# Optimization experiments

Measured on AMD Instinct MI355X. Metric: run time of the kernel, lower is better.

## Reference

```python
import jax, jax.numpy as jnp
import numpy as np

NUM_HEADS = 4
NUM_GROUPS = 8
EPS = 1e-5


def setup_inputs() -> dict:
    key = jax.random.key(0)
    ks = jax.random.split(key, 4)
    b, c, h, w = 16, 512, 32, 32
    x = jax.random.normal(ks[0], (b, c, h, w), dtype=jnp.float32)
    norm_gamma = jnp.ones((c,), dtype=jnp.float32)
    norm_beta = jnp.zeros((c,), dtype=jnp.float32)
    qkv_w = jax.random.normal(ks[1], (3 * c, c), dtype=jnp.float32) * (c ** -0.5)
    qkv_b = jnp.zeros((3 * c,), dtype=jnp.float32)
    proj_w = jax.random.normal(ks[2], (c, c), dtype=jnp.float32) * (c ** -0.5)
    proj_b = jnp.zeros((c,), dtype=jnp.float32)
    return {"x": x, "norm_gamma": norm_gamma, "norm_beta": norm_beta,
            "qkv_w": qkv_w, "qkv_b": qkv_b, "proj_w": proj_w, "proj_b": proj_b}


def reference(x, norm_gamma, norm_beta, qkv_w, qkv_b, proj_w, proj_b):
    b, c, h, w = x.shape
    nh = NUM_HEADS
    dh = c // nh
    n = h * w
    # GroupNorm(8, c): normalize over (c/G, h, w) within each group, biased var
    xg = x.reshape(b, NUM_GROUPS, -1)
    mu = jnp.mean(xg, axis=-1, keepdims=True)
    var = jnp.var(xg, axis=-1, keepdims=True)
    xn = ((xg - mu) * jax.lax.rsqrt(var + EPS)).reshape(b, c, h, w)
    xn = xn * norm_gamma[:, None, None] + norm_beta[:, None, None]
    # QKV 1x1 conv == channel matmul
    qkv = jnp.einsum('oc,bchw->bohw', qkv_w, xn) + qkv_b[:, None, None]
    q, k, v = jnp.split(qkv, 3, axis=1)  # each [b, c, h, w]

    def to_heads(t):  # [b, c, h, w] -> [b, nh, n, dh]
        return t.reshape(b, nh, dh, n).transpose(0, 1, 3, 2)

    q, k, v = to_heads(q), to_heads(k), to_heads(v)
    scale = dh ** -0.5
    attn = jax.nn.softmax(jnp.einsum('bhnd,bhmd->bhnm', q, k) * scale, axis=-1)
    out = jnp.einsum('bhnm,bhmd->bhnd', attn, v)  # [b, nh, n, dh]
    out = out.transpose(0, 1, 3, 2).reshape(b, c, h, w)
    out = jnp.einsum('oc,bchw->bohw', proj_w, out) + proj_b[:, None, None]
    return x + out
```

## Files before the change

kernel.cpp:

```cpp
#include <hip/hip_runtime.h>

typedef unsigned short u16;
typedef unsigned int   u32;

typedef __attribute__((ext_vector_type(8)))  short bf16x8;
typedef __attribute__((ext_vector_type(16))) float f32x16;
typedef __attribute__((ext_vector_type(2)))  unsigned int u32x2;
#define MFMA32(a, b, c) __builtin_amdgcn_mfma_f32_32x32x16_bf16(a, b, c, 0, 0, 0)

__device__ __forceinline__ float bf2f(u16 h) { return __uint_as_float(((u32)h) << 16); }
__device__ __forceinline__ u16 f2bf(float f) {
  u32 u = __float_as_uint(f);
  u += 0x7fffu + ((u >> 16) & 1u);
  return (u16)(u >> 16);
}
__device__ __forceinline__ void unpack8(uint4 u, float* f) {
  f[0] = __uint_as_float(u.x << 16); f[1] = __uint_as_float(u.x & 0xffff0000u);
  f[2] = __uint_as_float(u.y << 16); f[3] = __uint_as_float(u.y & 0xffff0000u);
  f[4] = __uint_as_float(u.z << 16); f[5] = __uint_as_float(u.z & 0xffff0000u);
  f[6] = __uint_as_float(u.w << 16); f[7] = __uint_as_float(u.w & 0xffff0000u);
}
__device__ __forceinline__ void unpack4(uint2 u, float* f) {
  f[0] = __uint_as_float(u.x << 16); f[1] = __uint_as_float(u.x & 0xffff0000u);
  f[2] = __uint_as_float(u.y << 16); f[3] = __uint_as_float(u.y & 0xffff0000u);
}

template <bool F>
__device__ __forceinline__ void load8(const void* p, size_t idx, float* f) {
  if constexpr (F) {
    const float4* q = (const float4*)((const float*)p + idx);
    float4 a = q[0], b = q[1];
    f[0] = a.x; f[1] = a.y; f[2] = a.z; f[3] = a.w;
    f[4] = b.x; f[5] = b.y; f[6] = b.z; f[7] = b.w;
  } else {
    unpack8(*(const uint4*)((const u16*)p + idx), f);
  }
}
template <bool F>
__device__ __forceinline__ void load4(const void* p, size_t idx, float* f) {
  if constexpr (F) {
    float4 a = *(const float4*)((const float*)p + idx);
    f[0] = a.x; f[1] = a.y; f[2] = a.z; f[3] = a.w;
  } else {
    unpack4(*(const uint2*)((const u16*)p + idx), f);
  }
}
template <bool F>
__device__ __forceinline__ float load1(const void* p, size_t idx) {
  if constexpr (F) return ((const float*)p)[idx];
  else return bf2f(((const u16*)p)[idx]);
}

__device__ __forceinline__ void gl2lds16(const void* g, void* l) {
  __builtin_amdgcn_global_load_lds(
      (const __attribute__((address_space(1))) void*)g,
      (__attribute__((address_space(3))) void*)l, 16, 0, 0);
}

__global__ void detect_dtype(const void* __restrict__ x, int* __restrict__ flag) {
  if (threadIdx.x == 0 && blockIdx.x == 0) {
    const u32* p = (const u32*)x;
    int sane = 0;
    for (int i = 0; i < 256; ++i) {
      u32 e = (p[i] >> 7) & 0xFFu;
      sane += (e >= 100u && e <= 150u) ? 1 : 0;
    }
    *flag = (sane < 192) ? 1 : 0;
  }
}

__global__ void signal_ws(u16* __restrict__ out, int n) {
  int i = blockIdx.x * 256 + threadIdx.x;
  if (i < n) out[i] = 0x42C8;
}

#define SM_SCALE 0.08838834764831843f
#define QSC 0.12751743f


template <bool F>
__global__ void __launch_bounds__(256) wconv(const void* __restrict__ qkvw,
                                             const void* __restrict__ qkvb,
                                             u16* __restrict__ dst,
                                             const int* __restrict__ flag) {
  if ((flag[0] != 0) != F) return;
  int i = blockIdx.x * 256 + threadIdx.x;
  if (i < 786432) {
    dst[i] = F ? f2bf(((const float*)qkvw)[i]) : ((const u16*)qkvw)[i];
  } else if (i < 787968) {
    int j = i - 786432;
    dst[i] = F ? f2bf(((const float*)qkvb)[j]) : ((const u16*)qkvb)[j];
  }
}

template <bool F>
__global__ void __launch_bounds__(256) gn_norm(const void* __restrict__ x,
                                               const void* __restrict__ gamma,
                                               const void* __restrict__ beta,
                                               u16* __restrict__ xT,
                                               const int* __restrict__ flag) {
  if ((flag[0] != 0) != F) return;
  const int g = blockIdx.x, b = blockIdx.y;
  const int tid = threadIdx.x;
  const size_t base = (size_t)(b * 512 + g * 64) * 1024;
  float sum = 0.f, sq = 0.f;
  for (int i = tid; i < 8192; i += 256) {
    float f[8]; load8<F>(x, base + (size_t)i * 8, f);
#pragma unroll
    for (int m = 0; m < 8; ++m) { sum += f[m]; sq += f[m] * f[m]; }
  }
  __shared__ float ssum[256], ssq[256];
  ssum[tid] = sum; ssq[tid] = sq; __syncthreads();
  for (int off = 128; off > 0; off >>= 1) {
    if (tid < off) { ssum[tid] += ssum[tid + off]; ssq[tid] += ssq[tid + off]; }
    __syncthreads();
  }
  __shared__ float scb[64], bsb[64];
  if (tid < 64) {
    float mu  = ssum[0] * (1.f / 65536.f);
    float var = ssq[0] * (1.f / 65536.f) - mu * mu;
    float s = load1<F>(gamma, g * 64 + tid) * rsqrtf(var + 1e-5f);
    scb[tid] = s;
    bsb[tid] = load1<F>(beta, g * 64 + tid) - mu * s;
  }
  __syncthreads();

  __shared__ float Tf[64][65];
  for (int s0 = 0; s0 < 1024; s0 += 64) {
#pragma unroll
    for (int half = 0; half < 2; ++half) {
      int idx = tid + half * 256;
      int c_loc = idx >> 3, s8 = (idx & 7) * 8;
      float f[8];
      load8<F>(x, base + (size_t)c_loc * 1024 + s0 + s8, f);
      float sm = scb[c_loc], ba = bsb[c_loc];
#pragma unroll
      for (int m = 0; m < 8; ++m) Tf[s8 + m][c_loc] = f[m] * sm + ba;
    }
    __syncthreads();
#pragma unroll
    for (int half = 0; half < 2; ++half) {
      int idx = tid + half * 256;
      int s_loc = idx >> 3, c8 = (idx & 7) * 8;
      u32 pk[4];
#pragma unroll
      for (int m = 0; m < 4; ++m)
        pk[m] = (u32)f2bf(Tf[s_loc][c8 + 2 * m]) |
                ((u32)f2bf(Tf[s_loc][c8 + 2 * m + 1]) << 16);
      *(uint4*)(xT + (size_t)(b * 1024 + s0 + s_loc) * 512 + g * 64 + c8) =
          make_uint4(pk[0], pk[1], pk[2], pk[3]);
    }
    __syncthreads();
  }
}

template <bool QSCALE, bool BIASN>
__global__ void __launch_bounds__(256, 4)
gemm_lds(const u16* __restrict__ A, const u16* __restrict__ B,
         const u16* __restrict__ bias, u16* __restrict__ outp,
         size_t aOff, size_t aBatch, size_t bBatch, int biasOff, size_t oBatch) {
  const int n0 = blockIdx.x * 128;
  const int m0 = blockIdx.y * 128;
  const int b  = blockIdx.z;
  __shared__ __align__(16) u16 At[8192];
  __shared__ __align__(16) u16 Bt[8192];
  const int tid = threadIdx.x;
  const int w = tid >> 6, lane = tid & 63;
  const int lo = lane & 31, hi = lane >> 5;
  const int wm = w >> 1, wn = w & 1;
  const u16* Ab = A + aOff + (size_t)b * aBatch;
  const u16* Bb = B + (size_t)b * bBatch;
  const int srow = lane >> 3, spc = lane & 7;

  f32x16 cA[2][2];
#pragma unroll
  for (int i = 0; i < 2; ++i)
#pragma unroll
    for (int j = 0; j < 2; ++j)
#pragma unroll
      for (int r = 0; r < 16; ++r) cA[i][j][r] = 0.f;

  for (int kt = 0; kt < 8; ++kt) {
    const int kb = kt * 64;
#pragma unroll
    for (int c = 0; c < 4; ++c) {
      int grp = w * 4 + c;
      int row = grp * 8 + srow;
      int lc  = spc ^ (row & 7);
      gl2lds16(Ab + (size_t)(m0 + row) * 512 + kb + lc * 8, &At[grp * 512]);
      gl2lds16(Bb + (size_t)(n0 + row) * 512 + kb + lc * 8, &Bt[grp * 512]);
    }
    __syncthreads();
#pragma unroll
    for (int k16 = 0; k16 < 4; ++k16) {
      const int lc = k16 * 2 + hi;
      const int rA0 = wm * 64 + lo,  rA1 = rA0 + 32;
      const int rB0 = wn * 64 + lo,  rB1 = rB0 + 32;
      bf16x8 a0 = *(const bf16x8*)&At[rA0 * 64 + ((lc ^ (rA0 & 7)) << 3)];
      bf16x8 a1 = *(const bf16x8*)&At[rA1 * 64 + ((lc ^ (rA1 & 7)) << 3)];
      bf16x8 b0 = *(const bf16x8*)&Bt[rB0 * 64 + ((lc ^ (rB0 & 7)) << 3)];
      bf16x8 b1 = *(const bf16x8*)&Bt[rB1 * 64 + ((lc ^ (rB1 & 7)) << 3)];
      cA[0][0] = MFMA32(a0, b0, cA[0][0]);
      cA[0][1] = MFMA32(a0, b1, cA[0][1]);
      cA[1][0] = MFMA32(a1, b0, cA[1][0]);
      cA[1][1] = MFMA32(a1, b1, cA[1][1]);
    }
    __syncthreads();
  }

  float bcol[2];
  if constexpr (BIASN) {
    bcol[0] = bf2f(bias[biasOff + n0 + wn * 64 + lo]);
    bcol[1] = bf2f(bias[biasOff + n0 + wn * 64 + 32 + lo]);
  }
#pragma unroll
  for (int mt = 0; mt < 2; ++mt)
#pragma unroll
    for (int nt = 0; nt < 2; ++nt) {
      const int nbase = n0 + wn * 64 + nt * 32;
      float scl = 1.f;
      if constexpr (QSCALE) scl = (nbase < 512) ? QSC : 1.f;
#pragma unroll
      for (int r = 0; r < 16; ++r) {
        int m = m0 + wm * 64 + mt * 32 + (r & 3) + 8 * (r >> 2) + 4 * hi;
        int n = nbase + lo;
        float v = cA[mt][nt][r];
        if constexpr (BIASN) v += bcol[nt];
        else                 v += bf2f(bias[biasOff + m]);
        if constexpr (QSCALE) v *= scl;
        outp[(size_t)b * oBatch + (size_t)m * 1024 + n] = f2bf(v);
      }
    }
}

template <bool F, bool AEXT, bool BEXT, bool BIASN, bool RESID, bool FOUT>
__global__ void __launch_bounds__(256, 4)
gemm_mfma(const void* __restrict__ A, const void* __restrict__ B,
          const void* __restrict__ bias, const void* __restrict__ resid,
          void* __restrict__ outp,
          size_t aOff, size_t bOff, int biasOff,
          size_t aBatch, size_t bBatch, size_t oBatch, size_t rBatch,
          const int* __restrict__ flag) {
  if ((flag[0] != 0) != F) return;
  const int n0 = blockIdx.x * 128;
  const int m0 = blockIdx.y * 128;
  const int b  = blockIdx.z;
  __shared__ __align__(16) u16 At[128][72];
  __shared__ __align__(16) u16 Bt[128][72];
  const int tid = threadIdx.x;
  const int w = tid >> 6, lane = tid & 63;
  const int lo = lane & 31, hi = lane >> 5;
  const int wm = w >> 1, wn = w & 1;
  const size_t aBase = aOff + (size_t)b * aBatch;
  const size_t bBase = bOff + (size_t)b * bBatch;

  f32x16 cA[2][2];
#pragma unroll
  for (int i = 0; i < 2; ++i)
#pragma unroll
    for (int j = 0; j < 2; ++j)
#pragma unroll
      for (int r = 0; r < 16; ++r) cA[i][j][r] = 0.f;

  for (int kt = 0; kt < 8; ++kt) {
#pragma unroll
    for (int i = 0; i < 4; ++i) {
      int idx = tid + i * 256;
      int row = idx >> 3, kc = (idx & 7) * 8;
      int k = kt * 64 + kc;
      {
        if constexpr (AEXT && F) {
          float f[8]; load8<true>(A, aBase + (size_t)(m0 + row) * 512 + k, f);
          u32 w0 = (u32)f2bf(f[0]) | ((u32)f2bf(f[1]) << 16);
          u32 w1 = (u32)f2bf(f[2]) | ((u32)f2bf(f[3]) << 16);
          u32 w2 = (u32)f2bf(f[4]) | ((u32)f2bf(f[5]) << 16);
          u32 w3 = (u32)f2bf(f[6]) | ((u32)f2bf(f[7]) << 16);
          *(uint4*)&At[row][kc] = make_uint4(w0, w1, w2, w3);
        } else {
          *(uint4*)&At[row][kc] =
              *(const uint4*)((const u16*)A + aBase + (size_t)(m0 + row) * 512 + k);
        }
      }
      {
        if constexpr (BEXT && F) {
          float f[8]; load8<true>(B, bBase + (size_t)(n0 + row) * 512 + k, f);
          u32 w0 = (u32)f2bf(f[0]) | ((u32)f2bf(f[1]) << 16);
          u32 w1 = (u32)f2bf(f[2]) | ((u32)f2bf(f[3]) << 16);
          u32 w2 = (u32)f2bf(f[4]) | ((u32)f2bf(f[5]) << 16);
          u32 w3 = (u32)f2bf(f[6]) | ((u32)f2bf(f[7]) << 16);
          *(uint4*)&Bt[row][kc] = make_uint4(w0, w1, w2, w3);
        } else {
          *(uint4*)&Bt[row][kc] =
              *(const uint4*)((const u16*)B + bBase + (size_t)(n0 + row) * 512 + k);
        }
      }
    }
    __syncthreads();
#pragma unroll
    for (int k16 = 0; k16 < 4; ++k16) {
      const int ko = k16 * 16 + hi * 8;
      bf16x8 a0 = *(const bf16x8*)&At[wm * 64 + lo][ko];
      bf16x8 a1 = *(const bf16x8*)&At[wm * 64 + 32 + lo][ko];
      bf16x8 b0 = *(const bf16x8*)&Bt[wn * 64 + lo][ko];
      bf16x8 b1 = *(const bf16x8*)&Bt[wn * 64 + 32 + lo][ko];
      cA[0][0] = MFMA32(a0, b0, cA[0][0]);
      cA[0][1] = MFMA32(a0, b1, cA[0][1]);
      cA[1][0] = MFMA32(a1, b0, cA[1][0]);
      cA[1][1] = MFMA32(a1, b1, cA[1][1]);
    }
    __syncthreads();
  }

  float bcol[2];
  if constexpr (BIASN) {
    bcol[0] = load1<F>(bias, biasOff + n0 + wn * 64 + lo);
    bcol[1] = load1<F>(bias, biasOff + n0 + wn * 64 + 32 + lo);
  }
#pragma unroll
  for (int mt = 0; mt < 2; ++mt)
#pragma unroll
    for (int nt = 0; nt < 2; ++nt) {
#pragma unroll
      for (int r = 0; r < 16; ++r) {
        int m = m0 + wm * 64 + mt * 32 + (r & 3) + 8 * (r >> 2) + 4 * hi;
        int n = n0 + wn * 64 + nt * 32 + lo;
        float v = cA[mt][nt][r];
        if constexpr (BIASN) v += bcol[nt];
        else                 v += load1<F>(bias, biasOff + m);
        if constexpr (RESID)
          v += load1<F>(resid, (size_t)b * rBatch + (size_t)m * 1024 + n);
        size_t off = (size_t)b * oBatch + (size_t)m * 1024 + n;
        if constexpr (FOUT) ((float*)outp)[off] = v;
        else                ((u16*)outp)[off] = f2bf(v);
      }
    }
}

__global__ void __launch_bounds__(256, 2) attn4(const u16* __restrict__ qkT,
                                                const u16* __restrict__ V,
                                                u16* __restrict__ aout) {
  const int bh = blockIdx.x;
  const int q0 = blockIdx.y * 128;
  const int b = bh >> 2, h = bh & 3;
  const u16* qt = qkT + (size_t)b * 1048576;
  const u16* vb = V + (size_t)b * 524288 + (size_t)(h * 128) * 1024;
  __shared__ __align__(16) u16 smem[32768];
  const int tid = threadIdx.x;
  const int w = tid >> 6, lane = tid & 63;
  const int lo = lane & 31, hi = lane >> 5;

#pragma unroll
  for (int c = 0; c < 8; ++c) {
    int grp = w * 8 + c;
    int row = grp * 4 + (lane >> 4);
    int lc  = (lane & 15) ^ (row & 7);
    gl2lds16(qt + (size_t)(q0 + row) * 1024 + h * 128 + lc * 8, &smem[grp * 512]);
  }
#pragma unroll
  for (int c = 0; c < 4; ++c) {
    int grp = w * 4 + c;
    { int row = grp * 4 + (lane >> 4);
      int lc  = (lane & 15) ^ (row & 7);
      gl2lds16(qt + (size_t)row * 1024 + 512 + h * 128 + lc * 8,
               &smem[16384 + grp * 512]); }
    { int row = grp * 8 + (lane >> 3);
      int lc  = (lane & 7) ^ (row & 7);
      gl2lds16(vb + (size_t)row * 1024 + lc * 8,
               &smem[16384 + 8192 + grp * 512]); }
  }
  __syncthreads();
  bf16x8 qf[8];
  {
    const int row = 32 * w + lo;
#pragma unroll
    for (int k16 = 0; k16 < 8; ++k16) {
      int lc = k16 * 2 + hi;
      qf[k16] = *(const bf16x8*)&smem[row * 128 + ((lc ^ (row & 7)) << 3)];
    }
  }
  __syncthreads();

  f32x16 o[4];
  float lp = 0.f;
#pragma unroll
  for (int dt = 0; dt < 4; ++dt)
#pragma unroll
    for (int r = 0; r < 16; ++r) o[dt][r] = 0.f;

  for (int kt = 0; kt < 16; ++kt) {
    const u16* rb = &smem[((kt & 1) ^ 1) << 14];
    u16* wbuf = &smem[(kt & 1) << 14];

    if (kt < 15) {
      const int k0n = (kt + 1) * 64;
#pragma unroll
      for (int c = 0; c < 4; ++c) {
        int grp = w * 4 + c;
        { int row = grp * 4 + (lane >> 4);
          int lc  = (lane & 15) ^ (row & 7);
          gl2lds16(qt + (size_t)(k0n + row) * 1024 + 512 + h * 128 + lc * 8,
                   wbuf + grp * 512); }
        { int row = grp * 8 + (lane >> 3);
          int lc  = (lane & 7) ^ (row & 7);
          gl2lds16(vb + (size_t)row * 1024 + k0n + lc * 8,
                   wbuf + 8192 + grp * 512); }
      }
    }

    f32x16 s0, s1;
#pragma unroll
    for (int r = 0; r < 16; ++r) { s0[r] = 0.f; s1[r] = 0.f; }
#pragma unroll
    for (int k16 = 0; k16 < 8; ++k16) {
      const int lc = k16 * 2 + hi;
      const int r0 = lo, r1 = lo + 32;
      bf16x8 kf0 = *(const bf16x8*)&rb[r0 * 128 + ((lc ^ (r0 & 7)) << 3)];
      bf16x8 kf1 = *(const bf16x8*)&rb[r1 * 128 + ((lc ^ (r1 & 7)) << 3)];
      s0 = MFMA32(kf0, qf[k16], s0);
      s1 = MFMA32(kf1, qf[k16], s1);
    }

#pragma unroll
    for (int r = 0; r < 16; ++r) {
      s0[r] = exp2f(s0[r]);
      s1[r] = exp2f(s1[r]);
      lp += s0[r] + s1[r];
    }

    bf16x8 pa[4];
#define MKPA(ps, rb0, dst) do {                                               \
      u32 qa0, qa1, qb0, qb1;                                                 \
      asm("v_cvt_pk_bf16_f32 %0, %1, %2" : "=v"(qa0)                          \
          : "v"((ps)[(rb0) + 0]), "v"((ps)[(rb0) + 1]));                      \
      asm("v_cvt_pk_bf16_f32 %0, %1, %2" : "=v"(qa1)                          \
          : "v"((ps)[(rb0) + 2]), "v"((ps)[(rb0) + 3]));                      \
      asm("v_cvt_pk_bf16_f32 %0, %1, %2" : "=v"(qb0)                          \
          : "v"((ps)[(rb0) + 4]), "v"((ps)[(rb0) + 5]));                      \
      asm("v_cvt_pk_bf16_f32 %0, %1, %2" : "=v"(qb1)                          \
          : "v"((ps)[(rb0) + 6]), "v"((ps)[(rb0) + 7]));                      \
      u32x2 r0 = __builtin_amdgcn_permlane32_swap(qa0, qb0, false, false);    \
      u32x2 r1 = __builtin_amdgcn_permlane32_swap(qa1, qb1, false, false);    \
      union { u32 u[4]; bf16x8 v8; } pk_;                                     \
      pk_.u[0] = r0[0]; pk_.u[1] = r1[0]; pk_.u[2] = r0[1]; pk_.u[3] = r1[1]; \
      dst = pk_.v8;                                                           \
    } while (0)
    MKPA(s0, 0, pa[0]);
    MKPA(s0, 8, pa[1]);
    MKPA(s1, 0, pa[2]);
    MKPA(s1, 8, pa[3]);
#undef MKPA

#pragma unroll
    for (int t = 0; t < 4; ++t) {
      const int lc = t * 2 + hi;
#pragma unroll
      for (int dt = 0; dt < 4; ++dt) {
        const int row = dt * 32 + lo;
        bf16x8 bv = *(const bf16x8*)&rb[8192 + row * 64 + ((lc ^ (row & 7)) << 3)];
        o[dt] = MFMA32(pa[t], bv, o[dt]);
      }
    }
    __syncthreads();
  }

  float linv = 1.f / (lp + __shfl_xor(lp, 32));
#pragma unroll
  for (int r = 0; r < 16; ++r) {
    int pat = (r & 3) + 8 * (r >> 2) + 4 * hi;
    float lr = __shfl(linv, pat);
    int q = q0 + 32 * w + pat;
    size_t base = (size_t)(b * 1024 + q) * 512 + h * 128;
    aout[base +  0 + lo] = f2bf(o[0][r] * lr);
    aout[base + 32 + lo] = f2bf(o[1][r] * lr);
    aout[base + 64 + lo] = f2bf(o[2][r] * lr);
    aout[base + 96 + lo] = f2bf(o[3][r] * lr);
  }
}


template <bool F>
__global__ void __launch_bounds__(256) gn_stats(const void* __restrict__ x,
                                                const void* __restrict__ gamma,
                                                const void* __restrict__ beta,
                                                float* __restrict__ sc,
                                                float* __restrict__ bs,
                                                const int* __restrict__ flag) {
  if ((flag[0] != 0) != F) return;
  const int g = blockIdx.x, b = blockIdx.y;
  const int tid = threadIdx.x;
  const size_t base = (size_t)(b * 512 + g * 64) * 1024;
  float sum = 0.f, sq = 0.f;
  for (int i = tid; i < 8192; i += 256) {
    float f[8]; load8<F>(x, base + (size_t)i * 8, f);
#pragma unroll
    for (int m = 0; m < 8; ++m) { sum += f[m]; sq += f[m] * f[m]; }
  }
  __shared__ float ssum[256], ssq[256];
  ssum[tid] = sum; ssq[tid] = sq; __syncthreads();
  for (int off = 128; off > 0; off >>= 1) {
    if (tid < off) { ssum[tid] += ssum[tid + off]; ssq[tid] += ssq[tid + off]; }
    __syncthreads();
  }
  if (tid < 64) {
    float mu  = ssum[0] * (1.f / 65536.f);
    float var = ssq[0] * (1.f / 65536.f) - mu * mu;
    int c = g * 64 + tid;
    float s = load1<F>(gamma, c) * rsqrtf(var + 1e-5f);
    sc[b * 512 + c] = s;
    bs[b * 512 + c] = load1<F>(beta, c) - mu * s;
  }
}

template <bool F, bool BEXT, bool FOUT>
__global__ void __launch_bounds__(256) gemm64(const void* __restrict__ A,
                                              const void* __restrict__ B,
                                              const float* __restrict__ sc,
                                              const float* __restrict__ bs,
                                              const void* __restrict__ bias,
                                              const void* __restrict__ resid,
                                              void* __restrict__ outp,
                                              int mrows, int donorm, int bstride,
                                              const int* __restrict__ flag) {
  if ((flag[0] != 0) != F) return;
  const int s0 = blockIdx.x * 64;
  const int o0 = blockIdx.y * 64;
  const int b  = blockIdx.z;
  __shared__ __align__(16) float At[64][36];
  __shared__ __align__(16) float Bt[64][36];
  const int tid = threadIdx.x;
  const int ty = tid >> 4, tx = tid & 15;
  const int i0 = ty * 4, j0 = tx * 4;
  const int arow = tid >> 2, akc = (tid & 3) * 8;
  const int brow = tid >> 3, bnc = (tid & 7) * 8;
  float acc[4][4] = {};

  for (int kt = 0; kt < 512; kt += 32) {
    float af[8];
    load8<F>(A, (size_t)(o0 + arow) * 512 + akc + kt, af);
    *(float4*)&At[arow][akc]     = make_float4(af[0], af[1], af[2], af[3]);
    *(float4*)&At[arow][akc + 4] = make_float4(af[4], af[5], af[6], af[7]);
    const int c = kt + brow;
    float bf[8];
    load8<(BEXT && F)>(B, (size_t)(b * bstride + c) * 1024 + s0 + bnc, bf);
    float smul = 1.f, badd = 0.f;
    if (donorm) { smul = sc[b * 512 + c]; badd = bs[b * 512 + c]; }
#pragma unroll
    for (int m = 0; m < 8; ++m) Bt[bnc + m][brow] = bf[m] * smul + badd;
    __syncthreads();
#pragma unroll
    for (int kq = 0; kq < 8; ++kq) {
      float4 a0 = *(const float4*)&At[i0 + 0][kq * 4];
      float4 a1 = *(const float4*)&At[i0 + 1][kq * 4];
      float4 a2 = *(const float4*)&At[i0 + 2][kq * 4];
      float4 a3 = *(const float4*)&At[i0 + 3][kq * 4];
      float4 c0 = *(const float4*)&Bt[j0 + 0][kq * 4];
      float4 c1 = *(const float4*)&Bt[j0 + 1][kq * 4];
      float4 c2 = *(const float4*)&Bt[j0 + 2][kq * 4];
      float4 c3 = *(const float4*)&Bt[j0 + 3][kq * 4];
#define DOT4(ii, jj, AV, CV) acc[ii][jj] += AV.x * CV.x + AV.y * CV.y + AV.z * CV.z + AV.w * CV.w;
      DOT4(0,0,a0,c0) DOT4(0,1,a0,c1) DOT4(0,2,a0,c2) DOT4(0,3,a0,c3)
      DOT4(1,0,a1,c0) DOT4(1,1,a1,c1) DOT4(1,2,a1,c2) DOT4(1,3,a1,c3)
      DOT4(2,0,a2,c0) DOT4(2,1,a2,c1) DOT4(2,2,a2,c2) DOT4(2,3,a2,c3)
      DOT4(3,0,a3,c0) DOT4(3,1,a3,c1) DOT4(3,2,a3,c2) DOT4(3,3,a3,c3)
#undef DOT4
    }
    __syncthreads();
  }
#pragma unroll
  for (int ii = 0; ii < 4; ++ii) {
    const int o = o0 + i0 + ii;
    const float bb = load1<F>(bias, o);
    float v[4];
#pragma unroll
    for (int jj = 0; jj < 4; ++jj) v[jj] = acc[ii][jj] + bb;
    if (resid) {
      float xf[4];
      load4<F>(resid, (size_t)(b * 512 + o) * 1024 + s0 + j0, xf);
#pragma unroll
      for (int jj = 0; jj < 4; ++jj) v[jj] += xf[jj];
    }
    const size_t ooff = (size_t)(b * mrows + o) * 1024 + s0 + j0;
    if constexpr (FOUT) {
      *(float4*)((float*)outp + ooff) = make_float4(v[0], v[1], v[2], v[3]);
    } else {
      uint2 pk;
      pk.x = (u32)f2bf(v[0]) | ((u32)f2bf(v[1]) << 16);
      pk.y = (u32)f2bf(v[2]) | ((u32)f2bf(v[3]) << 16);
      *(uint2*)((u16*)outp + ooff) = pk;
    }
  }
}

__global__ void __launch_bounds__(256, 2) attn_old(u16* __restrict__ qkv) {
  const int q0 = blockIdx.x * 128;
  const int bh = blockIdx.y;
  const int b = bh >> 2, h = bh & 3;
  u16* qp = qkv + (size_t)(b * 1536 + h * 128) * 1024;
  const u16* kp = qp + (size_t)512 * 1024;
  const u16* vp = qp + (size_t)1024 * 1024;
  __shared__ __align__(16) u16 Qt[128][136];
  __shared__ __align__(16) u16 Kt[32][136];
  __shared__ __align__(16) u16 Vt[128][40];
  __shared__ __align__(16) u16 Pt[128][40];
  const int tid = threadIdx.x;
  const int w = tid >> 6, lane = tid & 63;
  const int lo = lane & 31, hi = lane >> 5;

  for (int idx = tid; idx < 2048; idx += 256) {
    int d = idx >> 4, s8 = (idx & 15) * 8;
    uint4 qv = *(const uint4*)(qp + (size_t)d * 1024 + q0 + s8);
    const u16* qs = (const u16*)&qv;
#pragma unroll
    for (int m = 0; m < 8; ++m) Qt[s8 + m][d] = qs[m];
  }
  __syncthreads();
  bf16x8 qf[8];
#pragma unroll
  for (int kq = 0; kq < 8; ++kq)
    qf[kq] = *(const bf16x8*)&Qt[32 * w + lo][kq * 16 + hi * 8];

  f32x16 o0, o1, o2, o3;
  float lp[16];
#pragma unroll
  for (int r = 0; r < 16; ++r) { o0[r] = 0.f; o1[r] = 0.f; o2[r] = 0.f; o3[r] = 0.f; lp[r] = 0.f; }

  for (int kt = 0; kt < 32; ++kt) {
    const int k0 = kt * 32;
    __syncthreads();
    for (int idx = tid; idx < 512; idx += 256) {
      int d = idx >> 2, s8 = (idx & 3) * 8;
      uint4 kv = *(const uint4*)(kp + (size_t)d * 1024 + k0 + s8);
      const u16* ks = (const u16*)&kv;
#pragma unroll
      for (int m = 0; m < 8; ++m) Kt[s8 + m][d] = ks[m];
      *(uint4*)&Vt[d][s8] = *(const uint4*)(vp + (size_t)d * 1024 + k0 + s8);
    }
    __syncthreads();
    f32x16 acc;
#pragma unroll
    for (int r = 0; r < 16; ++r) acc[r] = 0.f;
#pragma unroll
    for (int kq = 0; kq < 8; ++kq) {
      bf16x8 bq = *(const bf16x8*)&Kt[lo][kq * 16 + hi * 8];
      acc = MFMA32(qf[kq], bq, acc);
    }
#pragma unroll
    for (int r = 0; r < 16; ++r) {
      float pe = __expf(acc[r] * SM_SCALE);
      lp[r] += pe;
      int row = (r & 3) + 8 * (r >> 2) + 4 * hi;
      Pt[32 * w + row][lo] = f2bf(pe);
    }
    __syncthreads();
#pragma unroll
    for (int kq2 = 0; kq2 < 2; ++kq2) {
      bf16x8 a2 = *(const bf16x8*)&Pt[32 * w + lo][kq2 * 16 + hi * 8];
      bf16x8 b0 = *(const bf16x8*)&Vt[ 0 + lo][kq2 * 16 + hi * 8];
      bf16x8 b1 = *(const bf16x8*)&Vt[32 + lo][kq2 * 16 + hi * 8];
      bf16x8 b2 = *(const bf16x8*)&Vt[64 + lo][kq2 * 16 + hi * 8];
      bf16x8 b3 = *(const bf16x8*)&Vt[96 + lo][kq2 * 16 + hi * 8];
      o0 = MFMA32(a2, b0, o0);
      o1 = MFMA32(a2, b1, o1);
      o2 = MFMA32(a2, b2, o2);
      o3 = MFMA32(a2, b3, o3);
    }
  }
#pragma unroll
  for (int r = 0; r < 16; ++r) {
    float su = lp[r];
    su += __shfl_xor(su, 1);  su += __shfl_xor(su, 2);
    su += __shfl_xor(su, 4);  su += __shfl_xor(su, 8);
    su += __shfl_xor(su, 16);
    float linv = 1.f / su;
    int row = (r & 3) + 8 * (r >> 2) + 4 * hi;
    int q = q0 + 32 * w + row;
    size_t base = (size_t)(b * 1536 + h * 128) * 1024 + q;
    qkv[base + (size_t)( 0 + lo) * 1024] = f2bf(o0[r] * linv);
    qkv[base + (size_t)(32 + lo) * 1024] = f2bf(o1[r] * linv);
    qkv[base + (size_t)(64 + lo) * 1024] = f2bf(o2[r] * linv);
    qkv[base + (size_t)(96 + lo) * 1024] = f2bf(o3[r] * linv);
  }
}

extern "C" void kernel_launch(void* const* d_in, const int* in_sizes, int n_in,
                              void* d_out, int out_size, void* d_ws, size_t ws_size,
                              hipStream_t stream) {
  const void* x     = d_in[0];
  const void* gamma = d_in[1];
  const void* beta  = d_in[2];
  const void* qkvw  = d_in[3];
  const void* qkvb  = d_in[4];
  const void* projw = d_in[5];
  const void* projb = d_in[6];

  char* ws = (char*)d_ws;
  const size_t MB = 1024 * 1024;
  const size_t FAST_NEED = 64 * MB + 64;
  const size_t OLD_NEED  = 48 * MB + 256 + 2 * 16 * 512 * 4;

  if (ws_size >= FAST_NEED) {
    u16* xT   = (u16*)ws;
    u16* qkT  = (u16*)(ws + 16 * MB);
    u16* Vbuf = (u16*)(ws + 48 * MB);
    int* flag = (int*)(ws + 64 * MB);
    u16* wbf  = (u16*)d_out;

    detect_dtype<<<1, 64, 0, stream>>>(x, flag);
    wconv<false><<<3078, 256, 0, stream>>>(qkvw, qkvb, wbf, flag);
    wconv<true ><<<3078, 256, 0, stream>>>(qkvw, qkvb, wbf, flag);
    gn_norm<false><<<dim3(8, 16), 256, 0, stream>>>(x, gamma, beta, xT, flag);
    gn_norm<true ><<<dim3(8, 16), 256, 0, stream>>>(x, gamma, beta, xT, flag);

    gemm_lds<true, true><<<dim3(8, 8, 16), 256, 0, stream>>>(
        xT, wbf, wbf + 786432, qkT, 0, 524288, 0, 0, 1048576);
    gemm_lds<false, false><<<dim3(8, 4, 16), 256, 0, stream>>>(
        wbf, xT, wbf + 786432, Vbuf, 524288, 0, 524288, 1024, 524288);

    attn4<<<dim3(64, 8), 256, 0, stream>>>(qkT, Vbuf, xT);

    gemm_mfma<false, true, false, false, true, false>
        <<<dim3(8, 4, 16), 256, 0, stream>>>(projw, xT, projb, x, d_out,
                                             0, 0, 0, 0, 524288, 524288, 524288, flag);
    gemm_mfma<true, true, false, false, true, true>
        <<<dim3(8, 4, 16), 256, 0, stream>>>(projw, xT, projb, x, d_out,
                                             0, 0, 0, 0, 524288, 524288, 524288, flag);
    return;
  }

  if (ws_size < OLD_NEED) {
    signal_ws<<<(out_size + 255) / 256, 256, 0, stream>>>((u16*)d_out, out_size);
    return;
  }

  const size_t QKV_BYTES = (size_t)16 * 1536 * 1024 * 2;
  u16* qkv  = (u16*)ws;
  int* flag = (int*)(ws + QKV_BYTES);
  float* sc = (float*)(ws + QKV_BYTES + 256);
  float* bs = sc + 16 * 512;

  detect_dtype<<<1, 64, 0, stream>>>(x, flag);
  gn_stats<false><<<dim3(8, 16), 256, 0, stream>>>(x, gamma, beta, sc, bs, flag);
  gn_stats<true ><<<dim3(8, 16), 256, 0, stream>>>(x, gamma, beta, sc, bs, flag);
  gemm64<false, true, false><<<dim3(16, 24, 16), 256, 0, stream>>>(
      qkvw, x, sc, bs, qkvb, nullptr, qkv, 1536, 1, 512, flag);
  gemm64<true, true, false><<<dim3(16, 24, 16), 256, 0, stream>>>(
      qkvw, x, sc, bs, qkvb, nullptr, qkv, 1536, 1, 512, flag);
  attn_old<<<dim3(8, 64), 256, 0, stream>>>(qkv);
  gemm64<false, false, false><<<dim3(16, 8, 16), 256, 0, stream>>>(
      projw, qkv, sc, bs, projb, x, d_out, 512, 0, 1536, flag);
  gemm64<true, false, true><<<dim3(16, 8, 16), 256, 0, stream>>>(
      projw, qkv, sc, bs, projb, x, d_out, 512, 0, 1536, flag);
}
```

Before: 257.7 us.

## Merge dtype-templated kernel pairs into runtime-dispatched launches and fuse QKV GEMMs

Replaces each pair of flag-gated template launches (wconv, gn_norm, proj) with a single kernel that branches on the dtype flag at runtime, removing the empty launches. The weight conversion is vectorised to 8 elements per thread. The two QKV GEMM launches become one grid where the upper blockIdx.y range computes V. The attention MFMA loops are wrapped in s_setprio raises. The costs are larger kernels with both dtype paths compiled in and extra runtime branching in the GEMM epilogue.

```diff
diff --git a/kernel.cpp b/kernel.cpp
--- a/kernel.cpp
+++ b/kernel.cpp
@@ -78,30 +78,37 @@
 #define QSC 0.12751743f
 
 
+__global__ void __launch_bounds__(256) wconv_rt(const void* __restrict__ qkvw,
+                                                const void* __restrict__ qkvb,
+                                                u16* __restrict__ dst,
+                                                const int* __restrict__ flag) {
+  const bool F = (flag[0] != 0);
+  int i = (blockIdx.x * 256 + threadIdx.x) * 8;
+  if (i >= 787968) return;
+  if (!F) {
+    uint4 v = (i < 786432) ? *(const uint4*)((const u16*)qkvw + i)
+                           : *(const uint4*)((const u16*)qkvb + (i - 786432));
+    *(uint4*)(dst + i) = v;
+  } else {
+    const float* src = (i < 786432) ? ((const float*)qkvw + i)
+                                    : ((const float*)qkvb + (i - 786432));
+    float f[8];
+    float4 a = *(const float4*)src, b = *(const float4*)(src + 4);
+    f[0]=a.x; f[1]=a.y; f[2]=a.z; f[3]=a.w; f[4]=b.x; f[5]=b.y; f[6]=b.z; f[7]=b.w;
+    u32 w0 = (u32)f2bf(f[0]) | ((u32)f2bf(f[1]) << 16);
+    u32 w1 = (u32)f2bf(f[2]) | ((u32)f2bf(f[3]) << 16);
+    u32 w2 = (u32)f2bf(f[4]) | ((u32)f2bf(f[5]) << 16);
+    u32 w3 = (u32)f2bf(f[6]) | ((u32)f2bf(f[7]) << 16);
+    *(uint4*)(dst + i) = make_uint4(w0, w1, w2, w3);
+  }
+}
+
 template <bool F>
-__global__ void __launch_bounds__(256) wconv(const void* __restrict__ qkvw,
-                                             const void* __restrict__ qkvb,
-                                             u16* __restrict__ dst,
-                                             const int* __restrict__ flag) {
-  if ((flag[0] != 0) != F) return;
-  int i = blockIdx.x * 256 + threadIdx.x;
-  if (i < 786432) {
-    dst[i] = F ? f2bf(((const float*)qkvw)[i]) : ((const u16*)qkvw)[i];
-  } else if (i < 787968) {
-    int j = i - 786432;
-    dst[i] = F ? f2bf(((const float*)qkvb)[j]) : ((const u16*)qkvb)[j];
-  }
-}
-
-template <bool F>
-__global__ void __launch_bounds__(256) gn_norm(const void* __restrict__ x,
-                                               const void* __restrict__ gamma,
-                                               const void* __restrict__ beta,
-                                               u16* __restrict__ xT,
-                                               const int* __restrict__ flag) {
-  if ((flag[0] != 0) != F) return;
-  const int g = blockIdx.x, b = blockIdx.y;
-  const int tid = threadIdx.x;
+__device__ __forceinline__ void gn_norm_body(
+    const void* __restrict__ x, const void* __restrict__ gamma,
+    const void* __restrict__ beta, u16* __restrict__ xT,
+    int g, int b, int tid,
+    float* ssum, float* ssq, float* scb, float* bsb, float (*Tf)[65]) {
   const size_t base = (size_t)(b * 512 + g * 64) * 1024;
   float sum = 0.f, sq = 0.f;
   for (int i = tid; i < 8192; i += 256) {
@@ -109,13 +116,11 @@
 #pragma unroll
     for (int m = 0; m < 8; ++m) { sum += f[m]; sq += f[m] * f[m]; }
   }
-  __shared__ float ssum[256], ssq[256];
   ssum[tid] = sum; ssq[tid] = sq; __syncthreads();
   for (int off = 128; off > 0; off >>= 1) {
     if (tid < off) { ssum[tid] += ssum[tid + off]; ssq[tid] += ssq[tid + off]; }
     __syncthreads();
   }
-  __shared__ float scb[64], bsb[64];
   if (tid < 64) {
     float mu  = ssum[0] * (1.f / 65536.f);
     float var = ssq[0] * (1.f / 65536.f) - mu * mu;
@@ -125,7 +130,6 @@
   }
   __syncthreads();
 
-  __shared__ float Tf[64][65];
   for (int s0 = 0; s0 < 1024; s0 += 64) {
 #pragma unroll
     for (int half = 0; half < 2; ++half) {
@@ -154,13 +158,24 @@
   }
 }
 
-template <bool QSCALE, bool BIASN>
+__global__ void __launch_bounds__(256) gn_norm_rt(const void* __restrict__ x,
+                                                  const void* __restrict__ gamma,
+                                                  const void* __restrict__ beta,
+                                                  u16* __restrict__ xT,
+                                                  const int* __restrict__ flag) {
+  __shared__ float ssum[256], ssq[256], scb[64], bsb[64];
+  __shared__ float Tf[64][65];
+  const int g = blockIdx.x, b = blockIdx.y, tid = threadIdx.x;
+  if (flag[0] != 0) gn_norm_body<true >(x, gamma, beta, xT, g, b, tid, ssum, ssq, scb, bsb, Tf);
+  else              gn_norm_body<false>(x, gamma, beta, xT, g, b, tid, ssum, ssq, scb, bsb, Tf);
+}
+
 __global__ void __launch_bounds__(256, 4)
-gemm_lds(const u16* __restrict__ A, const u16* __restrict__ B,
-         const u16* __restrict__ bias, u16* __restrict__ outp,
-         size_t aOff, size_t aBatch, size_t bBatch, int biasOff, size_t oBatch) {
+gemm_qkv(const u16* __restrict__ xT, const u16* __restrict__ wbf,
+         u16* __restrict__ qkT, u16* __restrict__ Vbuf) {
+  const bool vrole = (blockIdx.y >= 8);
   const int n0 = blockIdx.x * 128;
-  const int m0 = blockIdx.y * 128;
+  const int m0 = (vrole ? (int)blockIdx.y - 8 : (int)blockIdx.y) * 128;
   const int b  = blockIdx.z;
   __shared__ __align__(16) u16 At[8192];
   __shared__ __align__(16) u16 Bt[8192];
@@ -168,8 +183,10 @@
   const int w = tid >> 6, lane = tid & 63;
   const int lo = lane & 31, hi = lane >> 5;
   const int wm = w >> 1, wn = w & 1;
-  const u16* Ab = A + aOff + (size_t)b * aBatch;
-  const u16* Bb = B + (size_t)b * bBatch;
+  const u16* bias = wbf + 786432;
+  const u16* Ab = vrole ? (wbf + 524288) : (xT + (size_t)b * 524288);
+  const u16* Bb = vrole ? (xT + (size_t)b * 524288) : wbf;
+  u16* outp = vrole ? (Vbuf + (size_t)b * 524288) : (qkT + (size_t)b * 1048576);
   const int srow = lane >> 3, spc = lane & 7;
 
   f32x16 cA[2][2];
@@ -208,51 +225,44 @@
     __syncthreads();
   }
 
-  float bcol[2];
-  if constexpr (BIASN) {
-    bcol[0] = bf2f(bias[biasOff + n0 + wn * 64 + lo]);
-    bcol[1] = bf2f(bias[biasOff + n0 + wn * 64 + 32 + lo]);
+  float bcol[2] = {0.f, 0.f};
+  if (!vrole) {
+    bcol[0] = bf2f(bias[n0 + wn * 64 + lo]);
+    bcol[1] = bf2f(bias[n0 + wn * 64 + 32 + lo]);
   }
 #pragma unroll
   for (int mt = 0; mt < 2; ++mt)
 #pragma unroll
     for (int nt = 0; nt < 2; ++nt) {
       const int nbase = n0 + wn * 64 + nt * 32;
-      float scl = 1.f;
-      if constexpr (QSCALE) scl = (nbase < 512) ? QSC : 1.f;
 #pragma unroll
       for (int r = 0; r < 16; ++r) {
         int m = m0 + wm * 64 + mt * 32 + (r & 3) + 8 * (r >> 2) + 4 * hi;
         int n = nbase + lo;
         float v = cA[mt][nt][r];
-        if constexpr (BIASN) v += bcol[nt];
-        else                 v += bf2f(bias[biasOff + m]);
-        if constexpr (QSCALE) v *= scl;
-        outp[(size_t)b * oBatch + (size_t)m * 1024 + n] = f2bf(v);
+        if (!vrole) {
+          v += bcol[nt];
+          if (nbase < 512) v *= QSC;
+        } else {
+          v += bf2f(bias[1024 + m]);
+        }
+        outp[(size_t)m * 1024 + n] = f2bf(v);
       }
     }
 }
 
-template <bool F, bool AEXT, bool BEXT, bool BIASN, bool RESID, bool FOUT>
-__global__ void __launch_bounds__(256, 4)
-gemm_mfma(const void* __restrict__ A, const void* __restrict__ B,
-          const void* __restrict__ bias, const void* __restrict__ resid,
-          void* __restrict__ outp,
-          size_t aOff, size_t bOff, int biasOff,
-          size_t aBatch, size_t bBatch, size_t oBatch, size_t rBatch,
-          const int* __restrict__ flag) {
-  if ((flag[0] != 0) != F) return;
-  const int n0 = blockIdx.x * 128;
-  const int m0 = blockIdx.y * 128;
-  const int b  = blockIdx.z;
-  __shared__ __align__(16) u16 At[128][72];
-  __shared__ __align__(16) u16 Bt[128][72];
-  const int tid = threadIdx.x;
+template <bool F>
+__device__ __forceinline__ void proj_body(const void* __restrict__ A,
+                                          const u16* __restrict__ B,
+                                          const void* __restrict__ bias,
+                                          const void* __restrict__ resid,
+                                          void* __restrict__ outp,
+                                          int n0, int m0, int b, int tid,
+                                          u16 (*At)[72], u16 (*Bt)[72]) {
   const int w = tid >> 6, lane = tid & 63;
   const int lo = lane & 31, hi = lane >> 5;
   const int wm = w >> 1, wn = w & 1;
-  const size_t aBase = aOff + (size_t)b * aBatch;
-  const size_t bBase = bOff + (size_t)b * bBatch;
+  const size_t bBase = (size_t)b * 524288;
 
   f32x16 cA[2][2];
 #pragma unroll
@@ -269,8 +279,8 @@
       int row = idx >> 3, kc = (idx & 7) * 8;
       int k = kt * 64 + kc;
       {
-        if constexpr (AEXT && F) {
-          float f[8]; load8<true>(A, aBase + (size_t)(m0 + row) * 512 + k, f);
+        if constexpr (F) {
+          float f[8]; load8<true>(A, (size_t)(m0 + row) * 512 + k, f);
           u32 w0 = (u32)f2bf(f[0]) | ((u32)f2bf(f[1]) << 16);
           u32 w1 = (u32)f2bf(f[2]) | ((u32)f2bf(f[3]) << 16);
           u32 w2 = (u32)f2bf(f[4]) | ((u32)f2bf(f[5]) << 16);
@@ -278,22 +288,11 @@
           *(uint4*)&At[row][kc] = make_uint4(w0, w1, w2, w3);
         } else {
           *(uint4*)&At[row][kc] =
-              *(const uint4*)((const u16*)A + aBase + (size_t)(m0 + row) * 512 + k);
+              *(const uint4*)((const u16*)A + (size_t)(m0 + row) * 512 + k);
         }
       }
-      {
-        if constexpr (BEXT && F) {
-          float f[8]; load8<true>(B, bBase + (size_t)(n0 + row) * 512 + k, f);
-          u32 w0 = (u32)f2bf(f[0]) | ((u32)f2bf(f[1]) << 16);
-          u32 w1 = (u32)f2bf(f[2]) | ((u32)f2bf(f[3]) << 16);
-          u32 w2 = (u32)f2bf(f[4]) | ((u32)f2bf(f[5]) << 16);
-          u32 w3 = (u32)f2bf(f[6]) | ((u32)f2bf(f[7]) << 16);
-          *(uint4*)&Bt[row][kc] = make_uint4(w0, w1, w2, w3);
-        } else {
-          *(uint4*)&Bt[row][kc] =
-              *(const uint4*)((const u16*)B + bBase + (size_t)(n0 + row) * 512 + k);
-        }
-      }
+      *(uint4*)&Bt[row][kc] =
+          *(const uint4*)(B + bBase + (size_t)(n0 + row) * 512 + k);
     }
     __syncthreads();
 #pragma unroll
@@ -311,11 +310,6 @@
     __syncthreads();
   }
 
-  float bcol[2];
-  if constexpr (BIASN) {
-    bcol[0] = load1<F>(bias, biasOff + n0 + wn * 64 + lo);
-    bcol[1] = load1<F>(bias, biasOff + n0 + wn * 64 + 32 + lo);
-  }
 #pragma unroll
   for (int mt = 0; mt < 2; ++mt)
 #pragma unroll
@@ -325,15 +319,24 @@
         int m = m0 + wm * 64 + mt * 32 + (r & 3) + 8 * (r >> 2) + 4 * hi;
         int n = n0 + wn * 64 + nt * 32 + lo;
         float v = cA[mt][nt][r];
-        if constexpr (BIASN) v += bcol[nt];
-        else                 v += load1<F>(bias, biasOff + m);
-        if constexpr (RESID)
-          v += load1<F>(resid, (size_t)b * rBatch + (size_t)m * 1024 + n);
-        size_t off = (size_t)b * oBatch + (size_t)m * 1024 + n;
-        if constexpr (FOUT) ((float*)outp)[off] = v;
-        else                ((u16*)outp)[off] = f2bf(v);
+        v += load1<F>(bias, m);
+        v += load1<F>(resid, bBase + (size_t)m * 1024 + n);
+        size_t off = bBase + (size_t)m * 1024 + n;
+        if constexpr (F) ((float*)outp)[off] = v;
+        else             ((u16*)outp)[off] = f2bf(v);
       }
     }
+}
+
+__global__ void __launch_bounds__(256, 4)
+proj_rt(const void* __restrict__ projw, const u16* __restrict__ aout,
+        const void* __restrict__ projb, const void* __restrict__ x,
+        void* __restrict__ outp, const int* __restrict__ flag) {
+  __shared__ __align__(16) u16 At[128][72];
+  __shared__ __align__(16) u16 Bt[128][72];
+  const int n0 = blockIdx.x * 128, m0 = blockIdx.y * 128, b = blockIdx.z;
+  if (flag[0] != 0) proj_body<true >(projw, aout, projb, x, outp, n0, m0, b, threadIdx.x, At, Bt);
+  else              proj_body<false>(projw, aout, projb, x, outp, n0, m0, b, threadIdx.x, At, Bt);
 }
 
 __global__ void __launch_bounds__(256, 2) attn4(const u16* __restrict__ qkT,
@@ -410,6 +413,7 @@
     f32x16 s0, s1;
 #pragma unroll
     for (int r = 0; r < 16; ++r) { s0[r] = 0.f; s1[r] = 0.f; }
+    __builtin_amdgcn_s_setprio(1);
 #pragma unroll
     for (int k16 = 0; k16 < 8; ++k16) {
       const int lc = k16 * 2 + hi;
@@ -419,6 +423,7 @@
       s0 = MFMA32(kf0, qf[k16], s0);
       s1 = MFMA32(kf1, qf[k16], s1);
     }
+    __builtin_amdgcn_s_setprio(0);
 
 #pragma unroll
     for (int r = 0; r < 16; ++r) {
@@ -450,6 +455,7 @@
     MKPA(s1, 8, pa[3]);
 #undef MKPA
 
+    __builtin_amdgcn_s_setprio(1);
 #pragma unroll
     for (int t = 0; t < 4; ++t) {
       const int lc = t * 2 + hi;
@@ -460,6 +466,7 @@
         o[dt] = MFMA32(pa[t], bv, o[dt]);
       }
     }
+    __builtin_amdgcn_s_setprio(0);
     __syncthreads();
   }
 
@@ -706,24 +713,14 @@
     u16* wbf  = (u16*)d_out;
 
     detect_dtype<<<1, 64, 0, stream>>>(x, flag);
-    wconv<false><<<3078, 256, 0, stream>>>(qkvw, qkvb, wbf, flag);
-    wconv<true ><<<3078, 256, 0, stream>>>(qkvw, qkvb, wbf, flag);
-    gn_norm<false><<<dim3(8, 16), 256, 0, stream>>>(x, gamma, beta, xT, flag);
-    gn_norm<true ><<<dim3(8, 16), 256, 0, stream>>>(x, gamma, beta, xT, flag);
-
-    gemm_lds<true, true><<<dim3(8, 8, 16), 256, 0, stream>>>(
-        xT, wbf, wbf + 786432, qkT, 0, 524288, 0, 0, 1048576);
-    gemm_lds<false, false><<<dim3(8, 4, 16), 256, 0, stream>>>(
-        wbf, xT, wbf + 786432, Vbuf, 524288, 0, 524288, 1024, 524288);
+    wconv_rt<<<385, 256, 0, stream>>>(qkvw, qkvb, wbf, flag);
+    gn_norm_rt<<<dim3(8, 16), 256, 0, stream>>>(x, gamma, beta, xT, flag);
+
+    gemm_qkv<<<dim3(8, 12, 16), 256, 0, stream>>>(xT, wbf, qkT, Vbuf);
 
     attn4<<<dim3(64, 8), 256, 0, stream>>>(qkT, Vbuf, xT);
 
-    gemm_mfma<false, true, false, false, true, false>
-        <<<dim3(8, 4, 16), 256, 0, stream>>>(projw, xT, projb, x, d_out,
-                                             0, 0, 0, 0, 524288, 524288, 524288, flag);
-    gemm_mfma<true, true, false, false, true, true>
-        <<<dim3(8, 4, 16), 256, 0, stream>>>(projw, xT, projb, x, d_out,
-                                             0, 0, 0, 0, 524288, 524288, 524288, flag);
+    proj_rt<<<dim3(8, 4, 16), 256, 0, stream>>>(projw, xT, projb, x, d_out, flag);
     return;
   }
 
```

Result: no change. 254.0 us (-1.4%).
